# Kernel optimization log

Hardware: AMD Instinct MI355X
Metric: run time of the kernel (lower is better)

Reference implementation:

```python
import jax, jax.numpy as jnp
import numpy as np

N_NODES = 100000
N_EDGES = 3200000
D_IN = 256
D_OUT = 256


def setup_inputs() -> dict:
    key = jax.random.key(0)
    k1, k2, k3, k4, k5, k6 = jax.random.split(key, 6)
    X = jax.random.normal(k1, (N_NODES, D_IN), dtype=jnp.float32)
    edge_src = jax.random.randint(k2, (N_EDGES,), 0, N_NODES, dtype=jnp.int32)
    edge_dst = jax.random.randint(k3, (N_EDGES,), 0, N_NODES, dtype=jnp.int32)
    # nonnegative edge weights, as in a normalized adjacency
    edge_val = jax.random.uniform(k4, (N_EDGES,), dtype=jnp.float32)
    stdv = 1.0 / np.sqrt(D_OUT)
    W = jax.random.uniform(k5, (D_IN, D_OUT), minval=-stdv, maxval=stdv, dtype=jnp.float32)
    b = jax.random.uniform(k6, (D_OUT,), minval=-stdv, maxval=stdv, dtype=jnp.float32)
    return {"X": X, "edge_src": edge_src, "edge_dst": edge_dst, "edge_val": edge_val, "W": W, "b": b}


def reference(X, edge_src, edge_dst, edge_val, W, b):
    # support = X @ W  (dense GEMM, [N, D_OUT])
    support = X @ W
    # output = A @ support with A in COO form: gather rows at edge_src,
    # scale by edge weight, scatter-add into edge_dst rows.
    msgs = support[edge_src] * edge_val[:, None]          # [E, D_OUT]
    out = jax.ops.segment_sum(msgs, edge_dst, num_segments=N_NODES)
    return out + b
```

## Files before the change

### kernel.cpp

```cpp
#include <hip/hip_runtime.h>


typedef __bf16 bf16;
typedef bf16 bf16x4 __attribute__((ext_vector_type(4)));
typedef bf16 bf16x8 __attribute__((ext_vector_type(8)));
typedef float f32x4 __attribute__((ext_vector_type(4)));

#define D_DIM 256

__global__ void pack_w(const float* __restrict__ W, bf16* __restrict__ Wf) {
    int lane = threadIdx.x;
    int blk  = blockIdx.x;
    int kt = blk >> 4, nt = blk & 15;
    int t = lane & 15, q = lane >> 4;
    int krow = kt * 32 + q * 8;
    int col  = nt * 16 + t;
    bf16x8 v;
#pragma unroll
    for (int j = 0; j < 8; ++j)
        v[j] = (bf16)W[(size_t)(krow + j) * D_DIM + col];
    ((bf16x8*)Wf)[(size_t)blk * 64 + lane] = v;
}

__global__ void gemm_xw(const float* __restrict__ X, const bf16* __restrict__ Wf,
                        bf16* __restrict__ S, int N) {
    int wid  = blockIdx.x * 4 + (threadIdx.x >> 6);
    int base = wid * 16;
    if (base >= N) return;
    int lane = threadIdx.x & 63;
    int t = lane & 15, q = lane >> 4;

    const float* xrow = X + (size_t)(base + t) * D_DIM + q * 8;
    const bf16x8* wf = (const bf16x8*)Wf;

    f32x4 acc[16];
#pragma unroll
    for (int i = 0; i < 16; ++i) acc[i] = (f32x4){0.f, 0.f, 0.f, 0.f};

#pragma unroll
    for (int kt = 0; kt < 8; ++kt) {
        f32x4 x0 = *(const f32x4*)(xrow + kt * 32);
        f32x4 x1 = *(const f32x4*)(xrow + kt * 32 + 4);
        bf16x8 a;
        a[0] = (bf16)x0[0]; a[1] = (bf16)x0[1]; a[2] = (bf16)x0[2]; a[3] = (bf16)x0[3];
        a[4] = (bf16)x1[0]; a[5] = (bf16)x1[1]; a[6] = (bf16)x1[2]; a[7] = (bf16)x1[3];
#pragma unroll
        for (int nt = 0; nt < 16; ++nt) {
            bf16x8 bfr = wf[(size_t)(kt * 16 + nt) * 64 + lane];
            acc[nt] = __builtin_amdgcn_mfma_f32_16x16x32_bf16(a, bfr, acc[nt], 0, 0, 0);
        }
    }

#pragma unroll
    for (int nt = 0; nt < 16; ++nt) {
#pragma unroll
        for (int r = 0; r < 4; ++r) {
            S[(size_t)(base + q * 4 + r) * D_DIM + nt * 16 + t] = (bf16)acc[nt][r];
        }
    }
}

__global__ void rank_edges(const int* __restrict__ edst, int* __restrict__ counts,
                           int* __restrict__ erank, int E) {
    int E4 = E >> 2;
    const int4* d4 = (const int4*)edst;
    int4* r4 = (int4*)erank;
    int gid = blockIdx.x * blockDim.x + threadIdx.x;
    int stride = gridDim.x * blockDim.x;
    for (int i = gid; i < E4; i += stride) {
        int4 d = d4[i];
        int4 r;
        r.x = atomicAdd(&counts[d.x], 1);
        r.y = atomicAdd(&counts[d.y], 1);
        r.z = atomicAdd(&counts[d.z], 1);
        r.w = atomicAdd(&counts[d.w], 1);
        r4[i] = r;
    }
    if (gid < (E & 3)) {
        int e = E4 * 4 + gid;
        erank[e] = atomicAdd(&counts[edst[e]], 1);
    }
}

__global__ void scan_block(const int* __restrict__ counts, int n,
                           int* __restrict__ local_ex, int* __restrict__ bsums) {
    __shared__ int lds[1024];
    int tid = threadIdx.x;
    int g = blockIdx.x * 1024 + tid;
    int v = (g < n) ? counts[g] : 0;
    lds[tid] = v;
    __syncthreads();
    for (int d = 1; d < 1024; d <<= 1) {
        int add = (tid >= d) ? lds[tid - d] : 0;
        __syncthreads();
        lds[tid] += add;
        __syncthreads();
    }
    if (g < n) local_ex[g] = lds[tid] - v;
    if (tid == 1023) bsums[blockIdx.x] = lds[tid];
}

__global__ void scan_sums(const int* __restrict__ bsums, int nb, int* __restrict__ bex) {
    __shared__ int lds[128];
    int tid = threadIdx.x;
    int v = (tid < nb) ? bsums[tid] : 0;
    lds[tid] = v;
    __syncthreads();
    for (int d = 1; d < 128; d <<= 1) {
        int add = (tid >= d) ? lds[tid - d] : 0;
        __syncthreads();
        lds[tid] += add;
        __syncthreads();
    }
    if (tid < nb) bex[tid] = lds[tid] - v;
}

__global__ void add_base(int* __restrict__ off, const int* __restrict__ bex, int n) {
    int g = blockIdx.x * 1024 + threadIdx.x;
    if (g < n) off[g] += bex[blockIdx.x];
}

__global__ void scatter_edges(const int* __restrict__ esrc, const int* __restrict__ edst,
                              const float* __restrict__ evals, const int* __restrict__ erank,
                              const int* __restrict__ off, int2* __restrict__ eP, int E) {
    int E4 = E >> 2;
    const int4* s4 = (const int4*)esrc;
    const int4* d4 = (const int4*)edst;
    const float4* v4 = (const float4*)evals;
    const int4* r4 = (const int4*)erank;
    int gid = blockIdx.x * blockDim.x + threadIdx.x;
    int stride = gridDim.x * blockDim.x;
    for (int i = gid; i < E4; i += stride) {
        int4 s = s4[i];
        int4 d = d4[i];
        int4 r = r4[i];
        float4 v = v4[i];
        int2 p0 = {s.x, __float_as_int(v.x)};
        int2 p1 = {s.y, __float_as_int(v.y)};
        int2 p2 = {s.z, __float_as_int(v.z)};
        int2 p3 = {s.w, __float_as_int(v.w)};
        eP[off[d.x] + r.x] = p0;
        eP[off[d.y] + r.y] = p1;
        eP[off[d.z] + r.z] = p2;
        eP[off[d.w] + r.w] = p3;
    }
    if (gid < (E & 3)) {
        int e = E4 * 4 + gid;
        int2 p = {esrc[e], __float_as_int(evals[e])};
        eP[off[edst[e]] + erank[e]] = p;
    }
}

__global__ void __launch_bounds__(256) aggregate(
        const bf16* __restrict__ S, const int* __restrict__ off,
        const int* __restrict__ counts, const int2* __restrict__ eP,
        const float* __restrict__ b, float* __restrict__ out, int N) {
    int w = blockIdx.x * 4 + (threadIdx.x >> 6);
    if (w >= N) return;
    int lane = threadIdx.x & 63;

    f32x4 acc = ((const f32x4*)b)[lane];

    int e   = off[w];
    int end = e + counts[w];

    for (; e + 8 <= end; e += 8) {
        int2 r[8];
#pragma unroll
        for (int j = 0; j < 8; ++j) r[j] = eP[e + j];
        bf16x4 v[8];
#pragma unroll
        for (int j = 0; j < 8; ++j)
            v[j] = *((const bf16x4*)(S + (size_t)r[j].x * D_DIM) + lane);
#pragma unroll
        for (int j = 0; j < 8; ++j) {
            float wt = __int_as_float(r[j].y);
            acc[0] += wt * (float)v[j][0];
            acc[1] += wt * (float)v[j][1];
            acc[2] += wt * (float)v[j][2];
            acc[3] += wt * (float)v[j][3];
        }
    }
    for (; e < end; ++e) {
        int2 r = eP[e];
        float wt = __int_as_float(r.y);
        bf16x4 v = *((const bf16x4*)(S + (size_t)r.x * D_DIM) + lane);
        acc[0] += wt * (float)v[0];
        acc[1] += wt * (float)v[1];
        acc[2] += wt * (float)v[2];
        acc[3] += wt * (float)v[3];
    }
    ((f32x4*)out)[(size_t)w * 64 + lane] = acc;
}

extern "C" void kernel_launch(void* const* d_in, const int* in_sizes, int n_in,
                              void* d_out, int out_size, void* d_ws, size_t ws_size,
                              hipStream_t stream) {
    const float* X     = (const float*)d_in[0];
    const int*   esrc  = (const int*)d_in[1];
    const int*   edst  = (const int*)d_in[2];
    const float* evals = (const float*)d_in[3];
    const float* W     = (const float*)d_in[4];
    const float* bias  = (const float*)d_in[5];
    float* out = (float*)d_out;

    const int N = in_sizes[0] / D_DIM;
    const int E = in_sizes[1];

    auto alignup = [](size_t x) { return (x + 255) & ~(size_t)255; };
    char* ws = (char*)d_ws;
    size_t o = 0;
    bf16* S      = (bf16*)(ws + o); o = alignup(o + (size_t)N * D_DIM * sizeof(bf16));
    int* counts  = (int*)(ws + o);  o = alignup(o + (size_t)N * sizeof(int));
    int* off     = (int*)(ws + o);  o = alignup(o + (size_t)N * sizeof(int));
    int* erank   = (int*)(ws + o);  o = alignup(o + (size_t)E * sizeof(int));
    int* bsums   = (int*)(ws + o);  o = alignup(o + 1024 * sizeof(int));
    int* bex     = (int*)(ws + o);  o = alignup(o + 1024 * sizeof(int));
    int2* eP     = (int2*)(ws + o); o = alignup(o + (size_t)E * sizeof(int2));
    bf16* Wf     = (bf16*)(ws + o); o = alignup(o + (size_t)D_DIM * D_DIM * sizeof(bf16));

    const int nb = (N + 1023) / 1024;
    const int nwaves = (N + 15) / 16;

    hipMemsetAsync(counts, 0, (size_t)N * sizeof(int), stream);
    pack_w<<<128, 64, 0, stream>>>(W, Wf);
    gemm_xw<<<(nwaves + 3) / 4, 256, 0, stream>>>(X, Wf, S, N);
    rank_edges<<<2048, 256, 0, stream>>>(edst, counts, erank, E);
    scan_block<<<nb, 1024, 0, stream>>>(counts, N, off, bsums);
    scan_sums<<<1, 128, 0, stream>>>(bsums, nb, bex);
    add_base<<<nb, 1024, 0, stream>>>(off, bex, N);
    scatter_edges<<<2048, 256, 0, stream>>>(esrc, edst, evals, erank, off, eP, E);
    aggregate<<<(N + 3) / 4, 256, 0, stream>>>(S, off, counts, eP, bias, out, N);
}
```

Measured before the change: 676.2 us.

## Widen edge kernels to 8 per thread, add CSR end offset, deepen aggregate unroll

rank_edges and scatter_edges now use one thread per 8 edges with a full-size grid instead of a 2048-block grid-stride loop. This gives more independent atomics and loads in flight. A sentinel off[N]=E lets aggregate read its end offset directly instead of loading counts. Aggregate unrolls the gather to 16 edges with a 4-edge middle tail, and uses nontemporal loads for edge pairs and nontemporal stores for the output. The deeper unroll raises register pressure and may lower occupancy, and the streaming hints could change cache behaviour.

```diff
diff --git a/kernel.cpp b/kernel.cpp
--- a/kernel.cpp
+++ b/kernel.cpp
@@ -5,6 +5,7 @@
 typedef bf16 bf16x4 __attribute__((ext_vector_type(4)));
 typedef bf16 bf16x8 __attribute__((ext_vector_type(8)));
 typedef float f32x4 __attribute__((ext_vector_type(4)));
+typedef int i32x2 __attribute__((ext_vector_type(2)));
 
 #define D_DIM 256
 
@@ -62,23 +63,25 @@
 
 __global__ void rank_edges(const int* __restrict__ edst, int* __restrict__ counts,
                            int* __restrict__ erank, int E) {
-    int E4 = E >> 2;
-    const int4* d4 = (const int4*)edst;
-    int4* r4 = (int4*)erank;
-    int gid = blockIdx.x * blockDim.x + threadIdx.x;
-    int stride = gridDim.x * blockDim.x;
-    for (int i = gid; i < E4; i += stride) {
-        int4 d = d4[i];
-        int4 r;
-        r.x = atomicAdd(&counts[d.x], 1);
-        r.y = atomicAdd(&counts[d.y], 1);
-        r.z = atomicAdd(&counts[d.z], 1);
-        r.w = atomicAdd(&counts[d.w], 1);
-        r4[i] = r;
-    }
-    if (gid < (E & 3)) {
-        int e = E4 * 4 + gid;
-        erank[e] = atomicAdd(&counts[edst[e]], 1);
+    int gid  = blockIdx.x * blockDim.x + threadIdx.x;
+    int base = gid * 8;
+    if (base + 8 <= E) {
+        int4 d0 = *(const int4*)(edst + base);
+        int4 d1 = *(const int4*)(edst + base + 4);
+        int4 r0, r1;
+        r0.x = atomicAdd(&counts[d0.x], 1);
+        r0.y = atomicAdd(&counts[d0.y], 1);
+        r0.z = atomicAdd(&counts[d0.z], 1);
+        r0.w = atomicAdd(&counts[d0.w], 1);
+        r1.x = atomicAdd(&counts[d1.x], 1);
+        r1.y = atomicAdd(&counts[d1.y], 1);
+        r1.z = atomicAdd(&counts[d1.z], 1);
+        r1.w = atomicAdd(&counts[d1.w], 1);
+        *(int4*)(erank + base)     = r0;
+        *(int4*)(erank + base + 4) = r1;
+    } else {
+        for (int e = base; e < E; ++e)
+            erank[e] = atomicAdd(&counts[edst[e]], 1);
     }
 }
 
@@ -115,46 +118,54 @@
     if (tid < nb) bex[tid] = lds[tid] - v;
 }
 
-__global__ void add_base(int* __restrict__ off, const int* __restrict__ bex, int n) {
+__global__ void add_base(int* __restrict__ off, const int* __restrict__ bex,
+                         int n, int E) {
     int g = blockIdx.x * 1024 + threadIdx.x;
     if (g < n) off[g] += bex[blockIdx.x];
+    if (g == 0) off[n] = E;
 }
 
 __global__ void scatter_edges(const int* __restrict__ esrc, const int* __restrict__ edst,
                               const float* __restrict__ evals, const int* __restrict__ erank,
-                              const int* __restrict__ off, int2* __restrict__ eP, int E) {
-    int E4 = E >> 2;
-    const int4* s4 = (const int4*)esrc;
-    const int4* d4 = (const int4*)edst;
-    const float4* v4 = (const float4*)evals;
-    const int4* r4 = (const int4*)erank;
-    int gid = blockIdx.x * blockDim.x + threadIdx.x;
-    int stride = gridDim.x * blockDim.x;
-    for (int i = gid; i < E4; i += stride) {
-        int4 s = s4[i];
-        int4 d = d4[i];
-        int4 r = r4[i];
-        float4 v = v4[i];
-        int2 p0 = {s.x, __float_as_int(v.x)};
-        int2 p1 = {s.y, __float_as_int(v.y)};
-        int2 p2 = {s.z, __float_as_int(v.z)};
-        int2 p3 = {s.w, __float_as_int(v.w)};
-        eP[off[d.x] + r.x] = p0;
-        eP[off[d.y] + r.y] = p1;
-        eP[off[d.z] + r.z] = p2;
-        eP[off[d.w] + r.w] = p3;
-    }
-    if (gid < (E & 3)) {
-        int e = E4 * 4 + gid;
-        int2 p = {esrc[e], __float_as_int(evals[e])};
-        eP[off[edst[e]] + erank[e]] = p;
+                              const int* __restrict__ off, i32x2* __restrict__ eP, int E) {
+    int gid  = blockIdx.x * blockDim.x + threadIdx.x;
+    int base = gid * 8;
+    if (base + 8 <= E) {
+        int4 s0 = *(const int4*)(esrc + base);
+        int4 s1 = *(const int4*)(esrc + base + 4);
+        int4 d0 = *(const int4*)(edst + base);
+        int4 d1 = *(const int4*)(edst + base + 4);
+        int4 r0 = *(const int4*)(erank + base);
+        int4 r1 = *(const int4*)(erank + base + 4);
+        float4 v0 = *(const float4*)(evals + base);
+        float4 v1 = *(const float4*)(evals + base + 4);
+        int p0 = off[d0.x] + r0.x;
+        int p1 = off[d0.y] + r0.y;
+        int p2 = off[d0.z] + r0.z;
+        int p3 = off[d0.w] + r0.w;
+        int p4 = off[d1.x] + r1.x;
+        int p5 = off[d1.y] + r1.y;
+        int p6 = off[d1.z] + r1.z;
+        int p7 = off[d1.w] + r1.w;
+        eP[p0] = (i32x2){s0.x, __float_as_int(v0.x)};
+        eP[p1] = (i32x2){s0.y, __float_as_int(v0.y)};
+        eP[p2] = (i32x2){s0.z, __float_as_int(v0.z)};
+        eP[p3] = (i32x2){s0.w, __float_as_int(v0.w)};
+        eP[p4] = (i32x2){s1.x, __float_as_int(v1.x)};
+        eP[p5] = (i32x2){s1.y, __float_as_int(v1.y)};
+        eP[p6] = (i32x2){s1.z, __float_as_int(v1.z)};
+        eP[p7] = (i32x2){s1.w, __float_as_int(v1.w)};
+    } else {
+        for (int e = base; e < E; ++e) {
+            eP[off[edst[e]] + erank[e]] = (i32x2){esrc[e], __float_as_int(evals[e])};
+        }
     }
 }
 
 __global__ void __launch_bounds__(256) aggregate(
         const bf16* __restrict__ S, const int* __restrict__ off,
-        const int* __restrict__ counts, const int2* __restrict__ eP,
-        const float* __restrict__ b, float* __restrict__ out, int N) {
+        const i32x2* __restrict__ eP, const float* __restrict__ b,
+        float* __restrict__ out, int N) {
     int w = blockIdx.x * 4 + (threadIdx.x >> 6);
     if (w >= N) return;
     int lane = threadIdx.x & 63;
@@ -162,35 +173,52 @@
     f32x4 acc = ((const f32x4*)b)[lane];
 
     int e   = off[w];
-    int end = e + counts[w];
-
-    for (; e + 8 <= end; e += 8) {
-        int2 r[8];
-#pragma unroll
-        for (int j = 0; j < 8; ++j) r[j] = eP[e + j];
-        bf16x4 v[8];
-#pragma unroll
-        for (int j = 0; j < 8; ++j)
-            v[j] = *((const bf16x4*)(S + (size_t)r[j].x * D_DIM) + lane);
-#pragma unroll
-        for (int j = 0; j < 8; ++j) {
-            float wt = __int_as_float(r[j].y);
+    int end = off[w + 1];
+
+    for (; e + 16 <= end; e += 16) {
+        i32x2 r[16];
+#pragma unroll
+        for (int j = 0; j < 16; ++j) r[j] = __builtin_nontemporal_load(&eP[e + j]);
+        bf16x4 v[16];
+#pragma unroll
+        for (int j = 0; j < 16; ++j)
+            v[j] = *((const bf16x4*)(S + (size_t)r[j][0] * D_DIM) + lane);
+#pragma unroll
+        for (int j = 0; j < 16; ++j) {
+            float wt = __int_as_float(r[j][1]);
             acc[0] += wt * (float)v[j][0];
             acc[1] += wt * (float)v[j][1];
             acc[2] += wt * (float)v[j][2];
             acc[3] += wt * (float)v[j][3];
         }
     }
+    for (; e + 4 <= end; e += 4) {
+        i32x2 r[4];
+#pragma unroll
+        for (int j = 0; j < 4; ++j) r[j] = __builtin_nontemporal_load(&eP[e + j]);
+        bf16x4 v[4];
+#pragma unroll
+        for (int j = 0; j < 4; ++j)
+            v[j] = *((const bf16x4*)(S + (size_t)r[j][0] * D_DIM) + lane);
+#pragma unroll
+        for (int j = 0; j < 4; ++j) {
+            float wt = __int_as_float(r[j][1]);
+            acc[0] += wt * (float)v[j][0];
+            acc[1] += wt * (float)v[j][1];
+            acc[2] += wt * (float)v[j][2];
+            acc[3] += wt * (float)v[j][3];
+        }
+    }
     for (; e < end; ++e) {
-        int2 r = eP[e];
-        float wt = __int_as_float(r.y);
-        bf16x4 v = *((const bf16x4*)(S + (size_t)r.x * D_DIM) + lane);
+        i32x2 r = eP[e];
+        float wt = __int_as_float(r[1]);
+        bf16x4 v = *((const bf16x4*)(S + (size_t)r[0] * D_DIM) + lane);
         acc[0] += wt * (float)v[0];
         acc[1] += wt * (float)v[1];
         acc[2] += wt * (float)v[2];
         acc[3] += wt * (float)v[3];
     }
-    ((f32x4*)out)[(size_t)w * 64 + lane] = acc;
+    __builtin_nontemporal_store(acc, (f32x4*)out + (size_t)w * 64 + lane);
 }
 
 extern "C" void kernel_launch(void* const* d_in, const int* in_sizes, int n_in,
@@ -212,23 +240,24 @@
     size_t o = 0;
     bf16* S      = (bf16*)(ws + o); o = alignup(o + (size_t)N * D_DIM * sizeof(bf16));
     int* counts  = (int*)(ws + o);  o = alignup(o + (size_t)N * sizeof(int));
-    int* off     = (int*)(ws + o);  o = alignup(o + (size_t)N * sizeof(int));
+    int* off     = (int*)(ws + o);  o = alignup(o + (size_t)(N + 1) * sizeof(int));
     int* erank   = (int*)(ws + o);  o = alignup(o + (size_t)E * sizeof(int));
     int* bsums   = (int*)(ws + o);  o = alignup(o + 1024 * sizeof(int));
     int* bex     = (int*)(ws + o);  o = alignup(o + 1024 * sizeof(int));
-    int2* eP     = (int2*)(ws + o); o = alignup(o + (size_t)E * sizeof(int2));
+    i32x2* eP    = (i32x2*)(ws + o); o = alignup(o + (size_t)E * sizeof(i32x2));
     bf16* Wf     = (bf16*)(ws + o); o = alignup(o + (size_t)D_DIM * D_DIM * sizeof(bf16));
 
     const int nb = (N + 1023) / 1024;
     const int nwaves = (N + 15) / 16;
+    const int nthr8 = (E + 7) / 8;
 
     hipMemsetAsync(counts, 0, (size_t)N * sizeof(int), stream);
     pack_w<<<128, 64, 0, stream>>>(W, Wf);
     gemm_xw<<<(nwaves + 3) / 4, 256, 0, stream>>>(X, Wf, S, N);
-    rank_edges<<<2048, 256, 0, stream>>>(edst, counts, erank, E);
+    rank_edges<<<(nthr8 + 255) / 256, 256, 0, stream>>>(edst, counts, erank, E);
     scan_block<<<nb, 1024, 0, stream>>>(counts, N, off, bsums);
     scan_sums<<<1, 128, 0, stream>>>(bsums, nb, bex);
-    add_base<<<nb, 1024, 0, stream>>>(off, bex, N);
-    scatter_edges<<<2048, 256, 0, stream>>>(esrc, edst, evals, erank, off, eP, E);
-    aggregate<<<(N + 3) / 4, 256, 0, stream>>>(S, off, counts, eP, bias, out, N);
-}
+    add_base<<<nb, 1024, 0, stream>>>(off, bex, N, E);
+    scatter_edges<<<(nthr8 + 255) / 256, 256, 0, stream>>>(esrc, edst, evals, erank, off, eP, E);
+    aggregate<<<(N + 3) / 4, 256, 0, stream>>>(S, off, eP, bias, out, N);
+}
```

Result: no change. 664.2 us (-1.8%).
